# Kernel tuning notes

Measured on AMD Instinct MI355X. Metric: run time of the kernel, lower is better.

## Reference

```python
import jax, jax.numpy as jnp
import numpy as np

DIM_X = 100   # equation.dim_x
DIM_Y = 1     # equation.dim_y
DIM_D = 100   # equation.dim_d
DIM_H = 512   # dim_h
T_END = 1.0   # equation.T
BN_EPS = 1e-5
SQRT2 = float(np.sqrt(2.0))


def _linear_init(k, fan_in, fan_out):
    lim = 1.0 / np.sqrt(fan_in)
    kw, kb = jax.random.split(k)
    W = jax.random.uniform(kw, (fan_in, fan_out), minval=-lim, maxval=lim, dtype=jnp.float32)
    b = jax.random.uniform(kb, (fan_out,), minval=-lim, maxval=lim, dtype=jnp.float32)
    return W, b


def setup_inputs() -> dict:
    key = jax.random.key(0)
    ks = jax.random.split(key, 6)
    W1, b1 = _linear_init(ks[0], DIM_X + 1, DIM_H)
    W2, b2 = _linear_init(ks[1], DIM_H, DIM_H)
    W3, b3 = _linear_init(ks[2], DIM_H, DIM_H)
    W4, b4 = _linear_init(ks[3], DIM_H, DIM_Y * DIM_D)
    # y_0 = guess_y_0[0]*l + guess_y_0[1]*(1-l), l~U(0,1); guesses (0,1) -> y_0~U(0,1)
    y_0 = jax.random.uniform(ks[4], (DIM_Y,), dtype=jnp.float32)
    x_0 = jnp.zeros((DIM_X,), dtype=jnp.float32)  # equation.x_0
    g1 = jnp.ones((DIM_H,), jnp.float32); be1 = jnp.zeros((DIM_H,), jnp.float32)
    g2 = jnp.ones((DIM_H,), jnp.float32); be2 = jnp.zeros((DIM_H,), jnp.float32)
    return dict(y_0=y_0, W1=W1, b1=b1, W2=W2, b2=b2, W3=W3, b3=b3, W4=W4, b4=b4,
                g1=g1, be1=be1, g2=g2, be2=be2, x_0=x_0, batch_size=4096, N=64)


def reference(y_0, W1, b1, W2, b2, W3, b3, W4, b4, g1, be1, g2, be2, x_0, batch_size, N):
    dt = T_END / N
    sqrt_dt = float(np.sqrt(dt))

    def bn(h, g, be):  # training-mode BatchNorm1d: biased batch stats
        m = jnp.mean(h, axis=0)
        v = jnp.mean(jnp.square(h - m), axis=0)
        return g * (h - m) * jax.lax.rsqrt(v + BN_EPS) + be

    def get_z(x, t):
        h = jnp.concatenate([x, jnp.full((x.shape[0], 1), t, x.dtype)], axis=1)
        h = jax.nn.gelu(h @ W1 + b1, approximate=False)
        h = bn(jax.nn.gelu(h @ W2 + b2, approximate=False), g1, be1)
        h = bn(jax.nn.gelu(h @ W3 + b3, approximate=False), g2, be2)
        return (h @ W4 + b4).reshape(-1, DIM_Y, DIM_D)  # [B, dy, dd]

    x = jnp.broadcast_to(x_0, (batch_size, DIM_X))
    y = jnp.broadcast_to(y_0, (batch_size, DIM_Y))
    ts = jnp.arange(N, dtype=jnp.float32) * dt
    keys = jax.random.split(jax.random.key(42), N)

    def step(carry, inp):
        x, y = carry
        t, k = inp
        z = get_z(x, t)
        dW = jax.random.normal(k, (x.shape[0], DIM_D), dtype=x.dtype) * sqrt_dt
        # b(t,x,y)=0, sigma(t,x)=sqrt(2)*I  =>  x += sqrt(2)*dW
        x = x + SQRT2 * dW
        # f(t,x,y,z) = -0.5*||z||^2 (per dim_y row); z@dW contraction over dim_d
        f = -0.5 * jnp.sum(z * z, axis=2)                 # [B, dy]
        y = y - f * dt + jnp.einsum('byd,bd->by', z, dW)  # [B, dy]
        return (x, y), None

    (x, y), _ = jax.lax.scan(step, (x, y), (ts, keys))
    return x, y
```

## Files before the change

kernel.cpp:

```cpp
#include <hip/hip_runtime.h>
#include <hip/hip_bf16.h>
#include <stdint.h>

#define B 4096
#define DX 100
#define H 512
#define DD 100
#define NSTEPS 64
#define KIN 128
#define N4 128
#define NBLK 256
#define NTHR 512

typedef short bf8 __attribute__((ext_vector_type(8)));
typedef float f32x4 __attribute__((ext_vector_type(4)));

__device__ __forceinline__ ushort f2bf(float f) {
  union { __hip_bfloat16 h; ushort u; } cv;
  cv.h = __float2bfloat16(f);
  return cv.u;
}
__device__ __forceinline__ float bf2f(ushort h) {
  return __uint_as_float((uint32_t)h << 16);
}
__device__ __forceinline__ f32x4 mfma16(bf8 a, bf8 b, f32x4 c) {
  return __builtin_amdgcn_mfma_f32_16x16x32_bf16(a, b, c, 0, 0, 0);
}

__device__ __forceinline__ int aload_i(int* p) {
  return __hip_atomic_load(p, __ATOMIC_RELAXED, __HIP_MEMORY_SCOPE_AGENT);
}
__device__ __forceinline__ float aload_f(const float* p) {
  return __hip_atomic_load((float*)p, __ATOMIC_RELAXED, __HIP_MEMORY_SCOPE_AGENT);
}

__device__ __forceinline__ void tf2x32(uint32_t k0, uint32_t k1,
                                       uint32_t x0, uint32_t x1,
                                       uint32_t& o0, uint32_t& o1)
{
  uint32_t ks2 = 0x1BD11BDAu ^ k0 ^ k1;
  x0 += k0; x1 += k1;
#define RND(r) { x0 += x1; x1 = (x1 << (r)) | (x1 >> (32 - (r))); x1 ^= x0; }
  RND(13) RND(15) RND(26) RND(6)   x0 += k1;  x1 += ks2 + 1u;
  RND(17) RND(29) RND(16) RND(24)  x0 += ks2; x1 += k0  + 2u;
  RND(13) RND(15) RND(26) RND(6)   x0 += k0;  x1 += k1  + 3u;
  RND(17) RND(29) RND(16) RND(24)  x0 += k1;  x1 += ks2 + 4u;
  RND(13) RND(15) RND(26) RND(6)   x0 += ks2; x1 += k0  + 5u;
#undef RND
  o0 = x0; o1 = x1;
}
__device__ __forceinline__ void step_keys(int step, uint32_t& k0, uint32_t& k1)
{
  tf2x32(0u, 42u, 0u, (uint32_t)step, k0, k1);
}
__device__ __forceinline__ uint32_t jax_bits(uint32_t k0, uint32_t k1, uint32_t m)
{
  uint32_t a, b;
  tf2x32(k0, k1, 0u, m, a, b);
  return a ^ b;
}

__device__ __forceinline__ float jax_normal_from_bits(uint32_t bits)
{
  float f = __uint_as_float((bits >> 9) | 0x3f800000u) - 1.0f;
  const float lo = -0.99999994f;
  float u = fmaxf(lo, f * 2.0f + lo);
  float w = -log1pf(-u * u);
  float p;
  if (w < 5.0f) {
    w -= 2.5f;
    p =          2.81022636e-08f;
    p = fmaf(p, w, 3.43273939e-07f);
    p = fmaf(p, w, -3.5233877e-06f);
    p = fmaf(p, w, -4.39150654e-06f);
    p = fmaf(p, w, 0.00021858087f);
    p = fmaf(p, w, -0.00125372503f);
    p = fmaf(p, w, -0.00417768164f);
    p = fmaf(p, w, 0.246640727f);
    p = fmaf(p, w, 1.50140941f);
  } else {
    w = sqrtf(w) - 3.0f;
    p =          -0.000200214257f;
    p = fmaf(p, w, 0.000100950558f);
    p = fmaf(p, w, 0.00134934322f);
    p = fmaf(p, w, -0.00367342844f);
    p = fmaf(p, w, 0.00573950773f);
    p = fmaf(p, w, -0.0076224613f);
    p = fmaf(p, w, 0.00943887047f);
    p = fmaf(p, w, 1.00167406f);
    p = fmaf(p, w, 2.83297682f);
  }
  return 1.4142135623730951f * (p * u);
}

__device__ __forceinline__ float gelu(float v)
{
  float v2 = v * v;
  float zin = fmaf(0.044715f * v2, v, v);
  float z = fminf(1.5957691216057308f * zin, 80.0f);
  float e = __expf(z);
  float t = (e - 1.0f) * __builtin_amdgcn_rcpf(e + 1.0f);
  float hv = 0.5f * v;
  return fmaf(hv, t, hv);
}

__global__ void k_prep(const float* __restrict__ W1, const float* __restrict__ W2,
                       const float* __restrict__ W3, const float* __restrict__ W4,
                       ushort* __restrict__ w1t, ushort* __restrict__ w2t,
                       ushort* __restrict__ w3t, ushort* __restrict__ w4t)
{
  int gid = blockIdx.x * blockDim.x + threadIdx.x;
  int stride = gridDim.x * blockDim.x;
  for (int i = gid; i < H * KIN; i += stride) {
    int c = i >> 7, k = i & (KIN - 1);
    w1t[i] = f2bf(k < 101 ? W1[k * H + c] : 0.0f);
  }
  for (int i = gid; i < H * H; i += stride) {
    int c = i >> 9, k = i & (H - 1);
    w2t[i] = f2bf(W2[k * H + c]);
    w3t[i] = f2bf(W3[k * H + c]);
  }
  for (int i = gid; i < N4 * H; i += stride) {
    int c = i >> 9, k = i & (H - 1);
    w4t[i] = f2bf(c < DD ? W4[k * DD + c] : 0.0f);
  }
}


__global__ void k_init_chunk(const float* __restrict__ y0, const float* __restrict__ x0,
                             float* __restrict__ x_run, float* __restrict__ y,
                             float* __restrict__ bn)
{
  int gid = blockIdx.x * blockDim.x + threadIdx.x;
  int stride = gridDim.x * blockDim.x;
  for (int i = gid; i < B * DX; i += stride) x_run[i] = x0[i % DX];
  for (int i = gid; i < B; i += stride) y[i] = y0[0];
  for (int i = gid; i < NSTEPS * 4 * H; i += stride) bn[i] = 0.0f;
}

__global__ void k_xs(float* __restrict__ x_run, ushort* __restrict__ xs,
                     float* __restrict__ xout, int s0, int Sc)
{
  int gid = blockIdx.x * blockDim.x + threadIdx.x;
  int row = gid >> 7, col = gid & 127;
  const float dt = 1.0f / NSTEPS;
  if (col < DX) {
    float xr = x_run[row * DX + col];
    uint32_t m = (uint32_t)(row * DD + col);
    for (int t = 0; t < Sc; ++t) {
      xs[t * (B * KIN) + row * KIN + col] = f2bf(xr);
      uint32_t k0, k1;
      step_keys(s0 + t, k0, k1);
      float dW = 0.125f * jax_normal_from_bits(jax_bits(k0, k1, m));
      xr += 1.4142135623730951f * dW;
    }
    x_run[row * DX + col] = xr;
    if (s0 + Sc == NSTEPS) xout[row * DX + col] = xr;
  } else {
    for (int t = 0; t < Sc; ++t)
      xs[t * (B * KIN) + row * KIN + col] =
          (col == DX) ? f2bf((float)(s0 + t) * dt) : (ushort)0;
  }
}

__global__ __launch_bounds__(256, 3) void kL12(
    const ushort* __restrict__ xs, const ushort* __restrict__ w1t,
    const float* __restrict__ b1, const ushort* __restrict__ w2t,
    const float* __restrict__ b2, ushort* __restrict__ gb,
    float* __restrict__ bn, int s0)
{
  __shared__ ushort xt[64][136];
  __shared__ ushort at[64][264];
  const int tid = threadIdx.x;
  const int mb = blockIdx.x >> 1, nb = blockIdx.x & 1;
  const int base = mb * 64;
  float* bns = bn + (s0 + (mb >> 6)) * 4 * H;
  float* bnq = bns + H;
  const int w = tid >> 6, lane = tid & 63, lr = lane & 15, lg = lane >> 4;

  for (int i = tid; i < 64 * 16; i += 256) {
    int r = i >> 4, kk = (i & 15) * 8;
    *(bf8*)&xt[r][kk] = *(const bf8*)&xs[(base + r) * KIN + kk];
  }

  f32x4 acc[4][4];
#pragma unroll
  for (int mi = 0; mi < 4; mi++)
#pragma unroll
    for (int t = 0; t < 4; t++) acc[mi][t] = (f32x4)(0.0f);

#pragma unroll
  for (int c = 0; c < 2; c++) {
    __syncthreads();
#pragma unroll
    for (int tp = 0; tp < 2; tp++) {
      f32x4 a1[4][2];
#pragma unroll
      for (int mi = 0; mi < 4; mi++) { a1[mi][0] = (f32x4)(0.0f); a1[mi][1] = (f32x4)(0.0f); }
#pragma unroll
      for (int ks = 0; ks < 4; ks++) {
        bf8 af[4];
#pragma unroll
        for (int mi = 0; mi < 4; mi++)
          af[mi] = *(const bf8*)&xt[mi * 16 + lr][ks * 32 + lg * 8];
#pragma unroll
        for (int u = 0; u < 2; u++) {
          int hcol = c * 256 + w * 64 + (tp * 2 + u) * 16 + lr;
          bf8 b = *(const bf8*)(w1t + hcol * KIN + ks * 32 + lg * 8);
#pragma unroll
          for (int mi = 0; mi < 4; mi++) a1[mi][u] = mfma16(af[mi], b, a1[mi][u]);
        }
      }
#pragma unroll
      for (int u = 0; u < 2; u++) {
        int lcol = w * 64 + (tp * 2 + u) * 16 + lr;
        float bb = b1[c * 256 + lcol];
#pragma unroll
        for (int mi = 0; mi < 4; mi++)
#pragma unroll
          for (int r = 0; r < 4; r++)
            at[mi * 16 + lg * 4 + r][lcol] = f2bf(gelu(a1[mi][u][r] + bb));
      }
    }
    __syncthreads();
#pragma unroll
    for (int ks = 0; ks < 8; ks++) {
      bf8 af[4];
#pragma unroll
      for (int mi = 0; mi < 4; mi++)
        af[mi] = *(const bf8*)&at[mi * 16 + lr][ks * 32 + lg * 8];
#pragma unroll
      for (int t = 0; t < 4; t++) {
        int col = nb * 256 + w * 64 + t * 16 + lr;
        bf8 b = *(const bf8*)(w2t + col * H + c * 256 + ks * 32 + lg * 8);
#pragma unroll
        for (int mi = 0; mi < 4; mi++) acc[mi][t] = mfma16(af[mi], b, acc[mi][t]);
      }
    }
  }

#pragma unroll
  for (int t = 0; t < 4; t++) {
    int col = nb * 256 + w * 64 + t * 16 + lr;
    float bb = b2[col], s = 0.0f, q = 0.0f;
#pragma unroll
    for (int mi = 0; mi < 4; mi++)
#pragma unroll
      for (int r = 0; r < 4; r++) {
        float v = gelu(acc[mi][t][r] + bb);
        gb[(base + mi * 16 + lg * 4 + r) * H + col] = f2bf(v);
        s += v; q += v * v;
      }
    s += __shfl_xor(s, 16); s += __shfl_xor(s, 32);
    q += __shfl_xor(q, 16); q += __shfl_xor(q, 32);
    if (lane < 16) { unsafeAtomicAdd(&bns[col], s); unsafeAtomicAdd(&bnq[col], q); }
  }
}

__global__ __launch_bounds__(256, 3) void kL3(
    const ushort* __restrict__ gb, float* __restrict__ bn, int s0,
    const float* __restrict__ gamma, const float* __restrict__ beta,
    const ushort* __restrict__ w3t, const float* __restrict__ b3,
    ushort* __restrict__ ga)
{
  __shared__ float sc[H], sh[H];
  __shared__ ushort at[64][264];
  const int tid = threadIdx.x;
  const int mb = blockIdx.x >> 1, nb = blockIdx.x & 1;
  const int base = mb * 64;
  float* bn1s = bn + (s0 + (mb >> 6)) * 4 * H;
  float* bn1q = bn1s + H;
  float* bn2s = bn1s + 2 * H;
  float* bn2q = bn1s + 3 * H;
  const int w = tid >> 6, lane = tid & 63, lr = lane & 15, lg = lane >> 4;

  for (int c = tid; c < H; c += 256) {
    float m = bn1s[c] * (1.0f / B);
    float v = bn1q[c] * (1.0f / B) - m * m;
    float s2_ = gamma[c] * rsqrtf(v + 1e-5f);
    sc[c] = s2_; sh[c] = beta[c] - m * s2_;
  }

  f32x4 acc[4][4];
#pragma unroll
  for (int mi = 0; mi < 4; mi++)
#pragma unroll
    for (int t = 0; t < 4; t++) acc[mi][t] = (f32x4)(0.0f);

#pragma unroll
  for (int c = 0; c < 2; c++) {
    __syncthreads();
    for (int i = tid; i < 4096; i += 256) {
      int r = i >> 6, k4 = (i & 63) * 4, gk = c * 256 + k4;
      ushort4 gv = *(const ushort4*)&gb[(base + r) * H + gk];
      ushort4 o;
      o.x = f2bf(fmaf(bf2f(gv.x), sc[gk + 0], sh[gk + 0]));
      o.y = f2bf(fmaf(bf2f(gv.y), sc[gk + 1], sh[gk + 1]));
      o.z = f2bf(fmaf(bf2f(gv.z), sc[gk + 2], sh[gk + 2]));
      o.w = f2bf(fmaf(bf2f(gv.w), sc[gk + 3], sh[gk + 3]));
      *(ushort4*)&at[r][k4] = o;
    }
    __syncthreads();
#pragma unroll
    for (int ks = 0; ks < 8; ks++) {
      bf8 af[4];
#pragma unroll
      for (int mi = 0; mi < 4; mi++)
        af[mi] = *(const bf8*)&at[mi * 16 + lr][ks * 32 + lg * 8];
#pragma unroll
      for (int t = 0; t < 4; t++) {
        int col = nb * 256 + w * 64 + t * 16 + lr;
        bf8 b = *(const bf8*)(w3t + col * H + c * 256 + ks * 32 + lg * 8);
#pragma unroll
        for (int mi = 0; mi < 4; mi++) acc[mi][t] = mfma16(af[mi], b, acc[mi][t]);
      }
    }
  }

#pragma unroll
  for (int t = 0; t < 4; t++) {
    int col = nb * 256 + w * 64 + t * 16 + lr;
    float bb = b3[col], s = 0.0f, q = 0.0f;
#pragma unroll
    for (int mi = 0; mi < 4; mi++)
#pragma unroll
      for (int r = 0; r < 4; r++) {
        float v = gelu(acc[mi][t][r] + bb);
        ga[(base + mi * 16 + lg * 4 + r) * H + col] = f2bf(v);
        s += v; q += v * v;
      }
    s += __shfl_xor(s, 16); s += __shfl_xor(s, 32);
    q += __shfl_xor(q, 16); q += __shfl_xor(q, 32);
    if (lane < 16) { unsafeAtomicAdd(&bn2s[col], s); unsafeAtomicAdd(&bn2q[col], q); }
  }
}

__global__ __launch_bounds__(512, 2) void kL4(
    const ushort* __restrict__ ga, const float* __restrict__ bn, int s0,
    const float* __restrict__ gamma, const float* __restrict__ beta,
    const ushort* __restrict__ w4t, const float* __restrict__ b4,
    float* __restrict__ y)
{
  __shared__ float sc[H], sh[H];
  __shared__ ushort at[32 * 520];
  __shared__ float ys1[8][32], ys2[8][32];
  const int tid = threadIdx.x;
  const int sb = blockIdx.x >> 7;
  const int s = s0 + sb;
  const int lb = (blockIdx.x & 127) * 32;
  const int rbase = sb * B + lb;
  const float dt = 1.0f / NSTEPS;
  const float* bn2s = bn + s * 4 * H + 2 * H;
  const float* bn2q = bn2s + H;

  for (int c = tid; c < H; c += 512) {
    float m = bn2s[c] * (1.0f / B);
    float v = bn2q[c] * (1.0f / B) - m * m;
    float s2_ = gamma[c] * rsqrtf(v + 1e-5f);
    sc[c] = s2_; sh[c] = beta[c] - m * s2_;
  }
  __syncthreads();
  for (int i = tid; i < 32 * 128; i += 512) {
    int r = i >> 7, k4 = (i & 127) * 4;
    ushort4 gv = *(const ushort4*)&ga[(rbase + r) * H + k4];
    ushort4 o;
    o.x = f2bf(fmaf(bf2f(gv.x), sc[k4 + 0], sh[k4 + 0]));
    o.y = f2bf(fmaf(bf2f(gv.y), sc[k4 + 1], sh[k4 + 1]));
    o.z = f2bf(fmaf(bf2f(gv.z), sc[k4 + 2], sh[k4 + 2]));
    o.w = f2bf(fmaf(bf2f(gv.w), sc[k4 + 3], sh[k4 + 3]));
    *(ushort4*)&at[r * 520 + k4] = o;
  }
  __syncthreads();

  const int w = tid >> 6, lane = tid & 63, lr = lane & 15, lg = lane >> 4;
  const int col = w * 16 + lr;
  f32x4 acc[2];
  acc[0] = (f32x4)(0.0f); acc[1] = (f32x4)(0.0f);
#pragma unroll
  for (int ks = 0; ks < 16; ks++) {
    bf8 b = *(const bf8*)(w4t + col * H + ks * 32 + lg * 8);
#pragma unroll
    for (int mi = 0; mi < 2; mi++) {
      bf8 a = *(const bf8*)&at[(mi * 16 + lr) * 520 + ks * 32 + lg * 8];
      acc[mi] = mfma16(a, b, acc[mi]);
    }
  }

  uint32_t k0, k1;
  step_keys(s, k0, k1);
#pragma unroll
  for (int mi = 0; mi < 2; mi++) {
    float zz[4] = {0, 0, 0, 0}, zw[4] = {0, 0, 0, 0};
    if (col < DD) {
      float bb = b4[col];
#pragma unroll
      for (int r = 0; r < 4; r++) {
        int lrow = lb + mi * 16 + lg * 4 + r;
        float z = acc[mi][r] + bb;
        uint32_t m = (uint32_t)lrow * (uint32_t)DD + (uint32_t)col;
        float dW = 0.125f * jax_normal_from_bits(jax_bits(k0, k1, m));
        zz[r] = z * z;
        zw[r] = z * dW;
      }
    }
#pragma unroll
    for (int r = 0; r < 4; r++) {
      zz[r] += __shfl_xor(zz[r], 1); zz[r] += __shfl_xor(zz[r], 2);
      zz[r] += __shfl_xor(zz[r], 4); zz[r] += __shfl_xor(zz[r], 8);
      zw[r] += __shfl_xor(zw[r], 1); zw[r] += __shfl_xor(zw[r], 2);
      zw[r] += __shfl_xor(zw[r], 4); zw[r] += __shfl_xor(zw[r], 8);
    }
    if (lr == 0) {
#pragma unroll
      for (int r = 0; r < 4; r++) {
        ys1[w][mi * 16 + lg * 4 + r] = zz[r];
        ys2[w][mi * 16 + lg * 4 + r] = zw[r];
      }
    }
  }
  __syncthreads();
  if (tid < 32) {
    float s1 = 0.0f, s2_ = 0.0f;
#pragma unroll
    for (int i = 0; i < 8; i++) { s1 += ys1[i][tid]; s2_ += ys2[i][tid]; }
    unsafeAtomicAdd(&y[lb + tid], 0.5f * dt * s1 + s2_);
  }
}


__device__ __forceinline__ void gbar(int* cnt, int* gen, int mode)
{
  if (mode) __builtin_amdgcn_fence(__ATOMIC_RELEASE, "agent");
  __syncthreads();
  if (threadIdx.x == 0) {
    int g = aload_i(gen);
    int a = __hip_atomic_fetch_add(cnt, 1, __ATOMIC_RELAXED, __HIP_MEMORY_SCOPE_AGENT);
    if (a == NBLK - 1) {
      __hip_atomic_store(cnt, 0, __ATOMIC_RELAXED, __HIP_MEMORY_SCOPE_AGENT);
      __hip_atomic_store(gen, g + 1, __ATOMIC_RELAXED, __HIP_MEMORY_SCOPE_AGENT);
    } else {
      while (aload_i(gen) == g) __builtin_amdgcn_s_sleep(2);
    }
  }
  __syncthreads();
  if (mode) __builtin_amdgcn_fence(__ATOMIC_ACQUIRE, "agent");
  else      asm volatile("buffer_inv" ::: "memory");
}

__global__ void k_init_coop(const float* __restrict__ y0, const float* __restrict__ x0,
                            float* __restrict__ x, float* __restrict__ y,
                            float* __restrict__ bn, int* __restrict__ bar)
{
  int gid = blockIdx.x * blockDim.x + threadIdx.x;
  int stride = gridDim.x * blockDim.x;
  for (int i = gid; i < B * DX; i += stride) x[i] = x0[i % DX];
  for (int i = gid; i < B; i += stride) y[i] = y0[0];
  for (int i = gid; i < NSTEPS * 4 * H; i += stride) bn[i] = 0.0f;
  if (gid < 32) bar[gid] = 0;
}

__device__ __forceinline__ void l1_sec(const ushort* xt, const ushort* __restrict__ w1t,
                                       const float* __restrict__ b1,
                                       ushort* __restrict__ h1g,
                                       int base, int w, int lr, int lg)
{
  f32x4 a1[4];
#pragma unroll
  for (int t = 0; t < 4; t++) a1[t] = (f32x4)(0.0f);
#pragma unroll
  for (int ks = 0; ks < 4; ks++) {
    bf8 a = *(const bf8*)&xt[lr * 136 + ks * 32 + lg * 8];
#pragma unroll
    for (int t = 0; t < 4; t++) {
      int cc = w * 64 + t * 16 + lr;
      bf8 bfr = *(const bf8*)(w1t + cc * KIN + ks * 32 + lg * 8);
      a1[t] = mfma16(a, bfr, a1[t]);
    }
  }
#pragma unroll
  for (int t = 0; t < 4; t++) {
    int cc = w * 64 + t * 16 + lr;
    float bb = b1[cc];
#pragma unroll
    for (int r = 0; r < 4; r++)
      h1g[(base + lg * 4 + r) * H + cc] = f2bf(gelu(a1[t][r] + bb));
  }
}

__global__ void __launch_bounds__(NTHR, 2) k_steps(
    const ushort* __restrict__ w1t, const float* __restrict__ b1,
    const ushort* __restrict__ w2t, const float* __restrict__ b2,
    const ushort* __restrict__ w3t, const float* __restrict__ b3,
    const ushort* __restrict__ w4t, const float* __restrict__ b4,
    const float* __restrict__ ga1, const float* __restrict__ be1,
    const float* __restrict__ ga2, const float* __restrict__ be2,
    ushort* __restrict__ g1, ushort* __restrict__ g2h,
    float* __restrict__ bn, float* __restrict__ x, float* __restrict__ y,
    int* __restrict__ bar)
{
  __shared__ ushort smem[64 * 264];
  __shared__ float sc[H], sh[H];
  __shared__ float ys1[8][16], ys2[8][16];
  __shared__ int dsh[2];

  const int tid = threadIdx.x;
  const int w = tid >> 6, lane = tid & 63, lr = lane & 15, lg = lane >> 4;
  const float dt = 1.0f / NSTEPS;
  int* cnt = bar; int* gen = bar + 1;
  int* bins = bar + 2;
  int* gcnt = bar + 18;

  int sgs, mode;
  {
    if (tid == 0) {
      uint32_t xcc = __builtin_amdgcn_s_getreg(20 | (31 << 11)) & 15u;
      int j = __hip_atomic_fetch_add(&bins[xcc], 1, __ATOMIC_RELAXED, __HIP_MEMORY_SCOPE_AGENT);
      dsh[0] = (int)xcc; dsh[1] = j;
    }
    gbar(cnt, gen, 1);
    if (tid == 0) {
      int ok = 1;
      for (int k = 0; k < 8; k++)  ok &= (aload_i(&bins[k]) == 32);
      for (int k = 8; k < 16; k++) ok &= (aload_i(&bins[k]) == 0);
      if (ok) { dsh[0] = dsh[0] * 32 + dsh[1]; dsh[1] = 0; }
      else {
        dsh[0] = __hip_atomic_fetch_add(gcnt, 1, __ATOMIC_RELAXED, __HIP_MEMORY_SCOPE_AGENT);
        dsh[1] = 1;
      }
    }
    __syncthreads();
    sgs = dsh[0]; mode = dsh[1];
  }
  const int mb = sgs >> 2, q = sgs & 3;
  const int cbase = sgs * 16;

  {
    ushort* xt = smem;
    for (int i = tid; i < 16 * KIN; i += NTHR) {
      int r = i >> 7, k = i & (KIN - 1);
      xt[r * 136 + k] = (k < DX) ? f2bf(x[(cbase + r) * DX + k]) : (ushort)0;
    }
    __syncthreads();
    l1_sec(xt, w1t, b1, g2h, cbase, w, lr, lg);
  }
  gbar(cnt, gen, mode);

  for (int s = 0; s < NSTEPS; ++s) {
    float* bn1s = bn + s * 4 * H;
    float* bn1q = bn1s + H;
    float* bn2s = bn1s + 2 * H;
    float* bn2q = bn1s + 3 * H;

    {
      const int col = q * 128 + w * 16 + lr;
      f32x4 acc[4];
#pragma unroll
      for (int mi = 0; mi < 4; mi++) acc[mi] = (f32x4)(0.0f);
#pragma unroll
      for (int c = 0; c < 2; c++) {
        if (c) __syncthreads();
        for (int i = tid; i < 2048; i += NTHR) {
          int r = i >> 5, kk = (i & 31) * 8;
          *(bf8*)&smem[r * 264 + kk] = *(const bf8*)&g2h[(mb * 64 + r) * H + c * 256 + kk];
        }
        __syncthreads();
#pragma unroll
        for (int ks = 0; ks < 8; ks++) {
          bf8 b = *(const bf8*)(w2t + col * H + c * 256 + ks * 32 + lg * 8);
#pragma unroll
          for (int mi = 0; mi < 4; mi++) {
            bf8 a = *(const bf8*)&smem[(mi * 16 + lr) * 264 + ks * 32 + lg * 8];
            acc[mi] = mfma16(a, b, acc[mi]);
          }
        }
      }
      float bb = b2[col], ssum = 0.0f, qsum = 0.0f;
#pragma unroll
      for (int mi = 0; mi < 4; mi++)
#pragma unroll
        for (int r = 0; r < 4; r++) {
          float v = gelu(acc[mi][r] + bb);
          g1[(mb * 64 + mi * 16 + lg * 4 + r) * H + col] = f2bf(v);
          ssum += v; qsum += v * v;
        }
      ssum += __shfl_xor(ssum, 16); ssum += __shfl_xor(ssum, 32);
      qsum += __shfl_xor(qsum, 16); qsum += __shfl_xor(qsum, 32);
      if (lane < 16) { unsafeAtomicAdd(&bn1s[col], ssum); unsafeAtomicAdd(&bn1q[col], qsum); }
    }
    gbar(cnt, gen, mode);

    {
      const int col = q * 128 + w * 16 + lr;
      for (int c = tid; c < H; c += NTHR) {
        float m = aload_f(&bn1s[c]) * (1.0f / B);
        float v = aload_f(&bn1q[c]) * (1.0f / B) - m * m;
        float s2_ = ga1[c] * rsqrtf(v + 1e-5f);
        sc[c] = s2_; sh[c] = be1[c] - m * s2_;
      }
      __syncthreads();
      f32x4 acc[4];
#pragma unroll
      for (int mi = 0; mi < 4; mi++) acc[mi] = (f32x4)(0.0f);
#pragma unroll
      for (int c = 0; c < 2; c++) {
        if (c) __syncthreads();
        for (int i = tid; i < 4096; i += NTHR) {
          int r = i >> 6, k4 = (i & 63) * 4, gk = c * 256 + k4;
          ushort4 gv = *(const ushort4*)&g1[(mb * 64 + r) * H + gk];
          ushort4 o;
          o.x = f2bf(fmaf(bf2f(gv.x), sc[gk + 0], sh[gk + 0]));
          o.y = f2bf(fmaf(bf2f(gv.y), sc[gk + 1], sh[gk + 1]));
          o.z = f2bf(fmaf(bf2f(gv.z), sc[gk + 2], sh[gk + 2]));
          o.w = f2bf(fmaf(bf2f(gv.w), sc[gk + 3], sh[gk + 3]));
          *(ushort4*)&smem[r * 264 + k4] = o;
        }
        __syncthreads();
#pragma unroll
        for (int ks = 0; ks < 8; ks++) {
          bf8 b = *(const bf8*)(w3t + col * H + c * 256 + ks * 32 + lg * 8);
#pragma unroll
          for (int mi = 0; mi < 4; mi++) {
            bf8 a = *(const bf8*)&smem[(mi * 16 + lr) * 264 + ks * 32 + lg * 8];
            acc[mi] = mfma16(a, b, acc[mi]);
          }
        }
      }
      float bb = b3[col], ssum = 0.0f, qsum = 0.0f;
#pragma unroll
      for (int mi = 0; mi < 4; mi++)
#pragma unroll
        for (int r = 0; r < 4; r++) {
          float v = gelu(acc[mi][r] + bb);
          g2h[(mb * 64 + mi * 16 + lg * 4 + r) * H + col] = f2bf(v);
          ssum += v; qsum += v * v;
        }
      ssum += __shfl_xor(ssum, 16); ssum += __shfl_xor(ssum, 32);
      qsum += __shfl_xor(qsum, 16); qsum += __shfl_xor(qsum, 32);
      if (lane < 16) { unsafeAtomicAdd(&bn2s[col], ssum); unsafeAtomicAdd(&bn2q[col], qsum); }
    }
    gbar(cnt, gen, mode);

    {
      ushort* at16 = smem;
      ushort* xt   = smem + 16 * 520;
      for (int c = tid; c < H; c += NTHR) {
        float m = aload_f(&bn2s[c]) * (1.0f / B);
        float v = aload_f(&bn2q[c]) * (1.0f / B) - m * m;
        float s2_ = ga2[c] * rsqrtf(v + 1e-5f);
        sc[c] = s2_; sh[c] = be2[c] - m * s2_;
      }
      __syncthreads();
      for (int i = tid; i < 2048; i += NTHR) {
        int r = i >> 7, k4 = (i & 127) * 4;
        ushort4 gv = *(const ushort4*)&g2h[(cbase + r) * H + k4];
        ushort4 o;
        o.x = f2bf(fmaf(bf2f(gv.x), sc[k4 + 0], sh[k4 + 0]));
        o.y = f2bf(fmaf(bf2f(gv.y), sc[k4 + 1], sh[k4 + 1]));
        o.z = f2bf(fmaf(bf2f(gv.z), sc[k4 + 2], sh[k4 + 2]));
        o.w = f2bf(fmaf(bf2f(gv.w), sc[k4 + 3], sh[k4 + 3]));
        *(ushort4*)&at16[r * 520 + k4] = o;
      }
      __syncthreads();

      const int col = w * 16 + lr;
      f32x4 acc = (f32x4)(0.0f);
#pragma unroll
      for (int ks = 0; ks < 16; ks++) {
        bf8 a = *(const bf8*)&at16[lr * 520 + ks * 32 + lg * 8];
        bf8 b = *(const bf8*)(w4t + col * H + ks * 32 + lg * 8);
        acc = mfma16(a, b, acc);
      }

      uint32_t k0, k1;
      step_keys(s, k0, k1);
      float zz[4] = {0, 0, 0, 0}, zw[4] = {0, 0, 0, 0};
      float tnext = (float)(s + 1) * dt;
      if (col < DD) {
        float bb = b4[col];
#pragma unroll
        for (int r = 0; r < 4; r++) {
          int row = lg * 4 + r, grow = cbase + row;
          float z = acc[r] + bb;
          uint32_t m = (uint32_t)grow * (uint32_t)DD + (uint32_t)col;
          float dW = 0.125f * jax_normal_from_bits(jax_bits(k0, k1, m));
          float xn = x[grow * DX + col] + 1.4142135623730951f * dW;
          x[grow * DX + col] = xn;
          xt[row * 136 + col] = f2bf(xn);
          zz[r] = z * z;
          zw[r] = z * dW;
        }
      } else {
#pragma unroll
        for (int r = 0; r < 4; r++)
          xt[(lg * 4 + r) * 136 + col] = (col == DX) ? f2bf(tnext) : (ushort)0;
      }
#pragma unroll
      for (int r = 0; r < 4; r++) {
        zz[r] += __shfl_xor(zz[r], 1); zz[r] += __shfl_xor(zz[r], 2);
        zz[r] += __shfl_xor(zz[r], 4); zz[r] += __shfl_xor(zz[r], 8);
        zw[r] += __shfl_xor(zw[r], 1); zw[r] += __shfl_xor(zw[r], 2);
        zw[r] += __shfl_xor(zw[r], 4); zw[r] += __shfl_xor(zw[r], 8);
      }
      if (lr == 0) {
#pragma unroll
        for (int r = 0; r < 4; r++) {
          ys1[w][lg * 4 + r] = zz[r];
          ys2[w][lg * 4 + r] = zw[r];
        }
      }
      __syncthreads();
      if (tid < 16) {
        float s1 = 0.0f, s2_ = 0.0f;
#pragma unroll
        for (int i = 0; i < 8; i++) { s1 += ys1[i][tid]; s2_ += ys2[i][tid]; }
        y[cbase + tid] += 0.5f * dt * s1 + s2_;
      }
      if (s < NSTEPS - 1)
        l1_sec(xt, w1t, b1, g2h, cbase, w, lr, lg);
    }
    if (s < NSTEPS - 1) gbar(cnt, gen, mode);
  }
}


extern "C" void kernel_launch(void* const* d_in, const int* in_sizes, int n_in,
                              void* d_out, int out_size, void* d_ws, size_t ws_size,
                              hipStream_t stream)
{
  const float* y0  = (const float*)d_in[0];
  const float* W1  = (const float*)d_in[1];
  const float* b1  = (const float*)d_in[2];
  const float* W2  = (const float*)d_in[3];
  const float* b2  = (const float*)d_in[4];
  const float* W3  = (const float*)d_in[5];
  const float* b3  = (const float*)d_in[6];
  const float* W4  = (const float*)d_in[7];
  const float* b4  = (const float*)d_in[8];
  const float* ga1 = (const float*)d_in[9];
  const float* be1 = (const float*)d_in[10];
  const float* ga2 = (const float*)d_in[11];
  const float* be2 = (const float*)d_in[12];
  const float* x0  = (const float*)d_in[13];

  float* x = (float*)d_out;
  float* y = x + B * DX;

  const size_t fixed_b = (size_t)NSTEPS * 4 * H * 4 + (size_t)B * DX * 4 +
                         (size_t)(H * KIN + H * H + H * H + N4 * H) * 2;
  const size_t per_b = (size_t)B * H * 2 * 2;
  long smax = ((long)ws_size - (long)fixed_b) / (long)per_b;
  int S = (int)(smax < 64 ? smax : 64);

  if (S >= 1) {
    float* bn    = (float*)d_ws;
    float* x_run = bn + NSTEPS * 4 * H;
    ushort* w1t = (ushort*)(x_run + B * DX);
    ushort* w2t = w1t + H * KIN;
    ushort* w3t = w2t + H * H;
    ushort* w4t = w3t + H * H;
    ushort* ga  = w4t + N4 * H;
    ushort* gb  = ga + (size_t)S * B * H;
    ushort* xs  = ga;

    k_init_chunk<<<256, 256, 0, stream>>>(y0, x0, x_run, y, bn);
    k_prep<<<512, 256, 0, stream>>>(W1, W2, W3, W4, w1t, w2t, w3t, w4t);

    for (int s0 = 0; s0 < NSTEPS; s0 += S) {
      int Sc = (NSTEPS - s0 < S) ? (NSTEPS - s0) : S;
      k_xs<<<(B * KIN) / 256, 256, 0, stream>>>(x_run, xs, x, s0, Sc);
      kL12<<<Sc * 128, 256, 0, stream>>>(xs, w1t, b1, w2t, b2, gb, bn, s0);
      kL3 <<<Sc * 128, 256, 0, stream>>>(gb, bn, s0, ga1, be1, w3t, b3, ga);
      kL4 <<<Sc * 128, 512, 0, stream>>>(ga, bn, s0, ga2, be2, w4t, b4, y);
    }
  } else {
    int*   bar = (int*)d_ws;
    float* bn  = (float*)d_ws + 32;
    ushort* ub  = (ushort*)(bn + NSTEPS * 4 * H);
    ushort* g1  = ub;
    ushort* g2h = g1 + B * H;
    ushort* w1t = g2h + B * H;
    ushort* w2t = w1t + H * KIN;
    ushort* w3t = w2t + H * H;
    ushort* w4t = w3t + H * H;

    k_init_coop<<<256, 256, 0, stream>>>(y0, x0, x, y, bn, bar);
    k_prep<<<512, 256, 0, stream>>>(W1, W2, W3, W4, w1t, w2t, w3t, w4t);

    void* args[] = {
      (void*)&w1t, (void*)&b1, (void*)&w2t, (void*)&b2,
      (void*)&w3t, (void*)&b3, (void*)&w4t, (void*)&b4,
      (void*)&ga1, (void*)&be1, (void*)&ga2, (void*)&be2,
      (void*)&g1, (void*)&g2h, (void*)&bn, (void*)&x, (void*)&y, (void*)&bar
    };
    hipLaunchCooperativeKernel((const void*)k_steps, dim3(NBLK), dim3(NTHR),
                               args, 0, stream);
  }
}
```

Before: 1.397 ms.

## Use 512-thread blocks covering all 512 output columns in kL12 and kL3

kL12 and kL3 previously split each 64-row tile into two 256-thread blocks, one per half of the output columns. Each block had to recompute the full first layer (kL12) or redo the batch-norm staging of the input tile (kL3). Now a single 512-thread block with 8 waves covers all 512 columns, so the layer-1 GEMM, the GELU and the LDS staging are done once per row tile. The cost is half as many blocks, which may lower occupancy or latency hiding, and a tighter register budget under launch bounds of 512 threads with 4 blocks.

```diff
diff --git a/kernel.cpp b/kernel.cpp
--- a/kernel.cpp
+++ b/kernel.cpp
@@ -163,7 +163,7 @@
   }
 }
 
-__global__ __launch_bounds__(256, 3) void kL12(
+__global__ __launch_bounds__(512, 4) void kL12(
     const ushort* __restrict__ xs, const ushort* __restrict__ w1t,
     const float* __restrict__ b1, const ushort* __restrict__ w2t,
     const float* __restrict__ b2, ushort* __restrict__ gb,
@@ -172,13 +172,13 @@
   __shared__ ushort xt[64][136];
   __shared__ ushort at[64][264];
   const int tid = threadIdx.x;
-  const int mb = blockIdx.x >> 1, nb = blockIdx.x & 1;
+  const int mb = blockIdx.x;
   const int base = mb * 64;
   float* bns = bn + (s0 + (mb >> 6)) * 4 * H;
   float* bnq = bns + H;
   const int w = tid >> 6, lane = tid & 63, lr = lane & 15, lg = lane >> 4;
 
-  for (int i = tid; i < 64 * 16; i += 256) {
+  for (int i = tid; i < 64 * 16; i += 512) {
     int r = i >> 4, kk = (i & 15) * 8;
     *(bf8*)&xt[r][kk] = *(const bf8*)&xs[(base + r) * KIN + kk];
   }
@@ -193,34 +193,27 @@
   for (int c = 0; c < 2; c++) {
     __syncthreads();
 #pragma unroll
-    for (int tp = 0; tp < 2; tp++) {
-      f32x4 a1[4][2];
-#pragma unroll
-      for (int mi = 0; mi < 4; mi++) { a1[mi][0] = (f32x4)(0.0f); a1[mi][1] = (f32x4)(0.0f); }
+    for (int u = 0; u < 2; u++) {
+      f32x4 a1[4];
+#pragma unroll
+      for (int mi = 0; mi < 4; mi++) a1[mi] = (f32x4)(0.0f);
 #pragma unroll
       for (int ks = 0; ks < 4; ks++) {
-        bf8 af[4];
-#pragma unroll
-        for (int mi = 0; mi < 4; mi++)
-          af[mi] = *(const bf8*)&xt[mi * 16 + lr][ks * 32 + lg * 8];
-#pragma unroll
-        for (int u = 0; u < 2; u++) {
-          int hcol = c * 256 + w * 64 + (tp * 2 + u) * 16 + lr;
-          bf8 b = *(const bf8*)(w1t + hcol * KIN + ks * 32 + lg * 8);
-#pragma unroll
-          for (int mi = 0; mi < 4; mi++) a1[mi][u] = mfma16(af[mi], b, a1[mi][u]);
-        }
-      }
-#pragma unroll
-      for (int u = 0; u < 2; u++) {
-        int lcol = w * 64 + (tp * 2 + u) * 16 + lr;
-        float bb = b1[c * 256 + lcol];
-#pragma unroll
-        for (int mi = 0; mi < 4; mi++)
-#pragma unroll
-          for (int r = 0; r < 4; r++)
-            at[mi * 16 + lg * 4 + r][lcol] = f2bf(gelu(a1[mi][u][r] + bb));
-      }
+        int hcol = c * 256 + w * 32 + u * 16 + lr;
+        bf8 b = *(const bf8*)(w1t + hcol * KIN + ks * 32 + lg * 8);
+#pragma unroll
+        for (int mi = 0; mi < 4; mi++) {
+          bf8 a = *(const bf8*)&xt[mi * 16 + lr][ks * 32 + lg * 8];
+          a1[mi] = mfma16(a, b, a1[mi]);
+        }
+      }
+      int lcol = w * 32 + u * 16 + lr;
+      float bb = b1[c * 256 + lcol];
+#pragma unroll
+      for (int mi = 0; mi < 4; mi++)
+#pragma unroll
+        for (int r = 0; r < 4; r++)
+          at[mi * 16 + lg * 4 + r][lcol] = f2bf(gelu(a1[mi][r] + bb));
     }
     __syncthreads();
 #pragma unroll
@@ -231,7 +224,7 @@
         af[mi] = *(const bf8*)&at[mi * 16 + lr][ks * 32 + lg * 8];
 #pragma unroll
       for (int t = 0; t < 4; t++) {
-        int col = nb * 256 + w * 64 + t * 16 + lr;
+        int col = w * 64 + t * 16 + lr;
         bf8 b = *(const bf8*)(w2t + col * H + c * 256 + ks * 32 + lg * 8);
 #pragma unroll
         for (int mi = 0; mi < 4; mi++) acc[mi][t] = mfma16(af[mi], b, acc[mi][t]);
@@ -241,7 +234,7 @@
 
 #pragma unroll
   for (int t = 0; t < 4; t++) {
-    int col = nb * 256 + w * 64 + t * 16 + lr;
+    int col = w * 64 + t * 16 + lr;
     float bb = b2[col], s = 0.0f, q = 0.0f;
 #pragma unroll
     for (int mi = 0; mi < 4; mi++)
@@ -257,7 +250,7 @@
   }
 }
 
-__global__ __launch_bounds__(256, 3) void kL3(
+__global__ __launch_bounds__(512, 4) void kL3(
     const ushort* __restrict__ gb, float* __restrict__ bn, int s0,
     const float* __restrict__ gamma, const float* __restrict__ beta,
     const ushort* __restrict__ w3t, const float* __restrict__ b3,
@@ -266,7 +259,7 @@
   __shared__ float sc[H], sh[H];
   __shared__ ushort at[64][264];
   const int tid = threadIdx.x;
-  const int mb = blockIdx.x >> 1, nb = blockIdx.x & 1;
+  const int mb = blockIdx.x;
   const int base = mb * 64;
   float* bn1s = bn + (s0 + (mb >> 6)) * 4 * H;
   float* bn1q = bn1s + H;
@@ -274,7 +267,7 @@
   float* bn2q = bn1s + 3 * H;
   const int w = tid >> 6, lane = tid & 63, lr = lane & 15, lg = lane >> 4;
 
-  for (int c = tid; c < H; c += 256) {
+  for (int c = tid; c < H; c += 512) {
     float m = bn1s[c] * (1.0f / B);
     float v = bn1q[c] * (1.0f / B) - m * m;
     float s2_ = gamma[c] * rsqrtf(v + 1e-5f);
@@ -290,7 +283,7 @@
 #pragma unroll
   for (int c = 0; c < 2; c++) {
     __syncthreads();
-    for (int i = tid; i < 4096; i += 256) {
+    for (int i = tid; i < 4096; i += 512) {
       int r = i >> 6, k4 = (i & 63) * 4, gk = c * 256 + k4;
       ushort4 gv = *(const ushort4*)&gb[(base + r) * H + gk];
       ushort4 o;
@@ -309,7 +302,7 @@
         af[mi] = *(const bf8*)&at[mi * 16 + lr][ks * 32 + lg * 8];
 #pragma unroll
       for (int t = 0; t < 4; t++) {
-        int col = nb * 256 + w * 64 + t * 16 + lr;
+        int col = w * 64 + t * 16 + lr;
         bf8 b = *(const bf8*)(w3t + col * H + c * 256 + ks * 32 + lg * 8);
 #pragma unroll
         for (int mi = 0; mi < 4; mi++) acc[mi][t] = mfma16(af[mi], b, acc[mi][t]);
@@ -319,7 +312,7 @@
 
 #pragma unroll
   for (int t = 0; t < 4; t++) {
-    int col = nb * 256 + w * 64 + t * 16 + lr;
+    int col = w * 64 + t * 16 + lr;
     float bb = b3[col], s = 0.0f, q = 0.0f;
 #pragma unroll
     for (int mi = 0; mi < 4; mi++)
@@ -768,8 +761,8 @@
     for (int s0 = 0; s0 < NSTEPS; s0 += S) {
       int Sc = (NSTEPS - s0 < S) ? (NSTEPS - s0) : S;
       k_xs<<<(B * KIN) / 256, 256, 0, stream>>>(x_run, xs, x, s0, Sc);
-      kL12<<<Sc * 128, 256, 0, stream>>>(xs, w1t, b1, w2t, b2, gb, bn, s0);
-      kL3 <<<Sc * 128, 256, 0, stream>>>(gb, bn, s0, ga1, be1, w3t, b3, ga);
+      kL12<<<Sc * 64, 512, 0, stream>>>(xs, w1t, b1, w2t, b2, gb, bn, s0);
+      kL3 <<<Sc * 64, 512, 0, stream>>>(gb, bn, s0, ga1, be1, w3t, b3, ga);
       kL4 <<<Sc * 128, 512, 0, stream>>>(ga, bn, s0, ga2, be2, w4t, b4, y);
     }
   } else {
```

Measured after the change: 1.411 ms. About the same (+1.0%).

## Halve K-chunk size in L12/L3 to cut LDS and raise occupancy

Applied to the files above, without the earlier changes.

Splits the hidden-dimension K loop of the fused layer-1/2 and layer-3 kernels into four 128-wide chunks instead of two 256-wide ones. This halves the shared-memory activation tile. Layer-1 weight fragments are now preloaded into registers per column group. Launch bounds rise to 4 blocks per CU (and 4 for kL4) so more waves can hide latency, at the cost of more barriers and tighter register budgets that may cause spills. Index arithmetic is also widened to size_t.

```diff
diff --git a/kernel.cpp b/kernel.cpp
--- a/kernel.cpp
+++ b/kernel.cpp
@@ -163,14 +163,14 @@
   }
 }
 
-__global__ __launch_bounds__(256, 3) void kL12(
+__global__ __launch_bounds__(256, 4) void kL12(
     const ushort* __restrict__ xs, const ushort* __restrict__ w1t,
     const float* __restrict__ b1, const ushort* __restrict__ w2t,
     const float* __restrict__ b2, ushort* __restrict__ gb,
     float* __restrict__ bn, int s0)
 {
   __shared__ ushort xt[64][136];
-  __shared__ ushort at[64][264];
+  __shared__ ushort at[64][136];
   const int tid = threadIdx.x;
   const int mb = blockIdx.x >> 1, nb = blockIdx.x & 1;
   const int base = mb * 64;
@@ -180,8 +180,9 @@
 
   for (int i = tid; i < 64 * 16; i += 256) {
     int r = i >> 4, kk = (i & 15) * 8;
-    *(bf8*)&xt[r][kk] = *(const bf8*)&xs[(base + r) * KIN + kk];
-  }
+    *(bf8*)&xt[r][kk] = *(const bf8*)&xs[(size_t)(base + r) * KIN + kk];
+  }
+  __syncthreads();
 
   f32x4 acc[4][4];
 #pragma unroll
@@ -190,41 +191,37 @@
     for (int t = 0; t < 4; t++) acc[mi][t] = (f32x4)(0.0f);
 
 #pragma unroll
-  for (int c = 0; c < 2; c++) {
+  for (int c = 0; c < 4; c++) {
+    if (c) __syncthreads();
+#pragma unroll
+    for (int u = 0; u < 2; u++) {
+      int hcol = c * 128 + w * 32 + u * 16 + lr;
+      bf8 bfr[4];
+#pragma unroll
+      for (int ks = 0; ks < 4; ks++)
+        bfr[ks] = *(const bf8*)(w1t + hcol * KIN + ks * 32 + lg * 8);
+      f32x4 a1[4];
+#pragma unroll
+      for (int mi = 0; mi < 4; mi++) a1[mi] = (f32x4)(0.0f);
+#pragma unroll
+      for (int ks = 0; ks < 4; ks++) {
+#pragma unroll
+        for (int mi = 0; mi < 4; mi++) {
+          bf8 a = *(const bf8*)&xt[mi * 16 + lr][ks * 32 + lg * 8];
+          a1[mi] = mfma16(a, bfr[ks], a1[mi]);
+        }
+      }
+      int lcol = w * 32 + u * 16 + lr;
+      float bb = b1[c * 128 + lcol];
+#pragma unroll
+      for (int mi = 0; mi < 4; mi++)
+#pragma unroll
+        for (int r = 0; r < 4; r++)
+          at[mi * 16 + lg * 4 + r][lcol] = f2bf(gelu(a1[mi][r] + bb));
+    }
     __syncthreads();
 #pragma unroll
-    for (int tp = 0; tp < 2; tp++) {
-      f32x4 a1[4][2];
-#pragma unroll
-      for (int mi = 0; mi < 4; mi++) { a1[mi][0] = (f32x4)(0.0f); a1[mi][1] = (f32x4)(0.0f); }
-#pragma unroll
-      for (int ks = 0; ks < 4; ks++) {
-        bf8 af[4];
-#pragma unroll
-        for (int mi = 0; mi < 4; mi++)
-          af[mi] = *(const bf8*)&xt[mi * 16 + lr][ks * 32 + lg * 8];
-#pragma unroll
-        for (int u = 0; u < 2; u++) {
-          int hcol = c * 256 + w * 64 + (tp * 2 + u) * 16 + lr;
-          bf8 b = *(const bf8*)(w1t + hcol * KIN + ks * 32 + lg * 8);
-#pragma unroll
-          for (int mi = 0; mi < 4; mi++) a1[mi][u] = mfma16(af[mi], b, a1[mi][u]);
-        }
-      }
-#pragma unroll
-      for (int u = 0; u < 2; u++) {
-        int lcol = w * 64 + (tp * 2 + u) * 16 + lr;
-        float bb = b1[c * 256 + lcol];
-#pragma unroll
-        for (int mi = 0; mi < 4; mi++)
-#pragma unroll
-          for (int r = 0; r < 4; r++)
-            at[mi * 16 + lg * 4 + r][lcol] = f2bf(gelu(a1[mi][u][r] + bb));
-      }
-    }
-    __syncthreads();
-#pragma unroll
-    for (int ks = 0; ks < 8; ks++) {
+    for (int ks = 0; ks < 4; ks++) {
       bf8 af[4];
 #pragma unroll
       for (int mi = 0; mi < 4; mi++)
@@ -232,7 +229,7 @@
 #pragma unroll
       for (int t = 0; t < 4; t++) {
         int col = nb * 256 + w * 64 + t * 16 + lr;
-        bf8 b = *(const bf8*)(w2t + col * H + c * 256 + ks * 32 + lg * 8);
+        bf8 b = *(const bf8*)(w2t + col * H + c * 128 + ks * 32 + lg * 8);
 #pragma unroll
         for (int mi = 0; mi < 4; mi++) acc[mi][t] = mfma16(af[mi], b, acc[mi][t]);
       }
@@ -248,7 +245,7 @@
 #pragma unroll
       for (int r = 0; r < 4; r++) {
         float v = gelu(acc[mi][t][r] + bb);
-        gb[(base + mi * 16 + lg * 4 + r) * H + col] = f2bf(v);
+        gb[(size_t)(base + mi * 16 + lg * 4 + r) * H + col] = f2bf(v);
         s += v; q += v * v;
       }
     s += __shfl_xor(s, 16); s += __shfl_xor(s, 32);
@@ -257,14 +254,14 @@
   }
 }
 
-__global__ __launch_bounds__(256, 3) void kL3(
+__global__ __launch_bounds__(256, 4) void kL3(
     const ushort* __restrict__ gb, float* __restrict__ bn, int s0,
     const float* __restrict__ gamma, const float* __restrict__ beta,
     const ushort* __restrict__ w3t, const float* __restrict__ b3,
     ushort* __restrict__ ga)
 {
   __shared__ float sc[H], sh[H];
-  __shared__ ushort at[64][264];
+  __shared__ ushort at[64][136];
   const int tid = threadIdx.x;
   const int mb = blockIdx.x >> 1, nb = blockIdx.x & 1;
   const int base = mb * 64;
@@ -288,11 +285,11 @@
     for (int t = 0; t < 4; t++) acc[mi][t] = (f32x4)(0.0f);
 
 #pragma unroll
-  for (int c = 0; c < 2; c++) {
+  for (int c = 0; c < 4; c++) {
     __syncthreads();
-    for (int i = tid; i < 4096; i += 256) {
-      int r = i >> 6, k4 = (i & 63) * 4, gk = c * 256 + k4;
-      ushort4 gv = *(const ushort4*)&gb[(base + r) * H + gk];
+    for (int i = tid; i < 2048; i += 256) {
+      int r = i >> 5, k4 = (i & 31) * 4, gk = c * 128 + k4;
+      ushort4 gv = *(const ushort4*)&gb[(size_t)(base + r) * H + gk];
       ushort4 o;
       o.x = f2bf(fmaf(bf2f(gv.x), sc[gk + 0], sh[gk + 0]));
       o.y = f2bf(fmaf(bf2f(gv.y), sc[gk + 1], sh[gk + 1]));
@@ -302,7 +299,7 @@
     }
     __syncthreads();
 #pragma unroll
-    for (int ks = 0; ks < 8; ks++) {
+    for (int ks = 0; ks < 4; ks++) {
       bf8 af[4];
 #pragma unroll
       for (int mi = 0; mi < 4; mi++)
@@ -310,7 +307,7 @@
 #pragma unroll
       for (int t = 0; t < 4; t++) {
         int col = nb * 256 + w * 64 + t * 16 + lr;
-        bf8 b = *(const bf8*)(w3t + col * H + c * 256 + ks * 32 + lg * 8);
+        bf8 b = *(const bf8*)(w3t + col * H + c * 128 + ks * 32 + lg * 8);
 #pragma unroll
         for (int mi = 0; mi < 4; mi++) acc[mi][t] = mfma16(af[mi], b, acc[mi][t]);
       }
@@ -326,7 +323,7 @@
 #pragma unroll
       for (int r = 0; r < 4; r++) {
         float v = gelu(acc[mi][t][r] + bb);
-        ga[(base + mi * 16 + lg * 4 + r) * H + col] = f2bf(v);
+        ga[(size_t)(base + mi * 16 + lg * 4 + r) * H + col] = f2bf(v);
         s += v; q += v * v;
       }
     s += __shfl_xor(s, 16); s += __shfl_xor(s, 32);
@@ -335,7 +332,7 @@
   }
 }
 
-__global__ __launch_bounds__(512, 2) void kL4(
+__global__ __launch_bounds__(512, 4) void kL4(
     const ushort* __restrict__ ga, const float* __restrict__ bn, int s0,
     const float* __restrict__ gamma, const float* __restrict__ beta,
     const ushort* __restrict__ w4t, const float* __restrict__ b4,
@@ -362,7 +359,7 @@
   __syncthreads();
   for (int i = tid; i < 32 * 128; i += 512) {
     int r = i >> 7, k4 = (i & 127) * 4;
-    ushort4 gv = *(const ushort4*)&ga[(rbase + r) * H + k4];
+    ushort4 gv = *(const ushort4*)&ga[(size_t)(rbase + r) * H + k4];
     ushort4 o;
     o.x = f2bf(fmaf(bf2f(gv.x), sc[k4 + 0], sh[k4 + 0]));
     o.y = f2bf(fmaf(bf2f(gv.y), sc[k4 + 1], sh[k4 + 1]));
```

After: 1.433 ms. +2.6%, slower.
